# Kernel optimization log

Measured on AMD Instinct MI355X. Metric: run time of the kernel, lower is better.

Reference implementation:

```python
import jax, jax.numpy as jnp
import numpy as np

BATCH, SEQ, DIM = 4, 4096, 1024


def setup_inputs() -> dict:
    key = jax.random.key(0)
    ks = jax.random.split(key, 7)
    return {
        "x": jax.random.normal(ks[0], (BATCH, SEQ, DIM), dtype=jnp.float32),
        "hidden_r": jax.random.normal(ks[1], (BATCH, DIM), dtype=jnp.float32),
        "hidden_i": jax.random.normal(ks[2], (BATCH, DIM), dtype=jnp.float32),
        "phazor_r": jax.random.normal(ks[3], (DIM,), dtype=jnp.float32),
        "phazor_i": jax.random.normal(ks[4], (DIM,), dtype=jnp.float32),
        "phazor_init_r": jax.random.normal(ks[5], (DIM,), dtype=jnp.float32),
        "phazor_init_i": jax.random.normal(ks[6], (DIM,), dtype=jnp.float32),
    }


def reference(x, hidden_r, hidden_i, phazor_r, phazor_i, phazor_init_r, phazor_init_i):
    L = x.shape[1]
    phazor_p = phazor_r + 1j * phazor_i              # raw parameter, (dim,)
    phazor_init = phazor_init_r + 1j * phazor_init_i  # (dim,)
    hidden = hidden_r + 1j * hidden_i                 # (batch, dim)

    mag = jnp.abs(phazor_p)
    phazor = phazor_p / mag * jnp.exp(-mag)           # unit-direction * exp(-|p|), (dim,)

    # (len, dim): phazor ** t for t in [0, len)
    t = jnp.arange(L)[:, None]
    phazor_prog = phazor[None, :] ** t

    filt = phazor_prog * phazor_init[None, :]         # (len, dim)
    filt_fft = jnp.fft.fft(filt, n=2 * L, axis=0)     # (2len, dim)
    x_fft = jnp.fft.fft(x.astype(jnp.complex64), n=2 * L, axis=1)  # (batch, 2len, dim)

    conv = jnp.fft.ifft(filt_fft[None, :, :] * x_fft, axis=1)[:, :L, :]  # (batch, len, dim)

    out = conv + hidden[:, None, :] * phazor_prog[None, :, :] * phazor[None, None, :]
    return out
```

## Files before the change

kernel.cpp:

```cpp
#include <hip/hip_runtime.h>
#include <math.h>

#define BATCH 4
#define SEQ   4096
#define DIM   1024
#define VEC   4

typedef float f32x4 __attribute__((ext_vector_type(4)));

__device__ __forceinline__ void load_params4(
    const float* __restrict__ phr, const float* __restrict__ phi,
    const float* __restrict__ pir, const float* __restrict__ pii,
    int d0, float* ar, float* ai, float* br, float* bi)
{
    float4 p_r = *reinterpret_cast<const float4*>(phr + d0);
    float4 p_i = *reinterpret_cast<const float4*>(phi + d0);
    float4 q_r = *reinterpret_cast<const float4*>(pir + d0);
    float4 q_i = *reinterpret_cast<const float4*>(pii + d0);
    float prv[VEC] = {p_r.x, p_r.y, p_r.z, p_r.w};
    float piv[VEC] = {p_i.x, p_i.y, p_i.z, p_i.w};
    float qrv[VEC] = {q_r.x, q_r.y, q_r.z, q_r.w};
    float qiv[VEC] = {q_i.x, q_i.y, q_i.z, q_i.w};
#pragma unroll
    for (int j = 0; j < VEC; ++j) {
        float mag = sqrtf(prv[j] * prv[j] + piv[j] * piv[j]);
        float s = expf(-mag) / mag;
        ar[j] = prv[j] * s;
        ai[j] = piv[j] * s;
        br[j] = qrv[j];
        bi[j] = qiv[j];
    }
}

template <int NC>
__global__ __launch_bounds__(256, 4) void k_carry(
    const float* __restrict__ x,
    const float* __restrict__ phr, const float* __restrict__ phi,
    const float* __restrict__ pir, const float* __restrict__ pii,
    float2* __restrict__ carry)
{
    constexpr int S = SEQ / NC;
    const int d0 = (blockIdx.x * blockDim.x + threadIdx.x) * VEC;
    const int c = blockIdx.y, b = blockIdx.z;

    float ar[VEC], ai[VEC], br[VEC], bi[VEC];
    load_params4(phr, phi, pir, pii, d0, ar, ai, br, bi);

    const float* xp = x + ((size_t)b * SEQ + (size_t)c * S) * DIM + d0;
    float Cr[VEC] = {0.f, 0.f, 0.f, 0.f};
    float Ci[VEC] = {0.f, 0.f, 0.f, 0.f};
#pragma unroll 4
    for (int t = 0; t < S; ++t) {
        float4 xv = *reinterpret_cast<const float4*>(xp + (size_t)t * DIM);
        float xa[VEC] = {xv.x, xv.y, xv.z, xv.w};
#pragma unroll
        for (int j = 0; j < VEC; ++j) {
            float nr = fmaf(ar[j], Cr[j], fmaf(-ai[j], Ci[j], br[j] * xa[j]));
            float ni = fmaf(ar[j], Ci[j], fmaf( ai[j], Cr[j], bi[j] * xa[j]));
            Cr[j] = nr; Ci[j] = ni;
        }
    }
    float2* cp = carry + ((size_t)b * NC + c) * DIM + d0;
#pragma unroll
    for (int j = 0; j < VEC; ++j) cp[j] = make_float2(Cr[j], Ci[j]);
}

template <int NC>
__global__ __launch_bounds__(64) void k_prefix(
    const float* __restrict__ phr, const float* __restrict__ phi,
    const float* __restrict__ hr,  const float* __restrict__ hi_,
    const float2* __restrict__ carry,
    float2* __restrict__ prefix)
{
    constexpr int S = SEQ / NC;
    const int idx = blockIdx.x * blockDim.x + threadIdx.x;
    const int b = idx / DIM, d = idx % DIM;

    float pr = phr[d], pi = phi[d];
    float mag = sqrtf(pr * pr + pi * pi);
    float sc = expf(-mag) / mag;
    float ar = pr * sc, ai = pi * sc;

    float Ar = 1.f, Ai = 0.f, sr = ar, si = ai;
    int e = S;
    while (e) {
        if (e & 1) {
            float nr = Ar * sr - Ai * si;
            Ai = Ar * si + Ai * sr;
            Ar = nr;
        }
        float nr = sr * sr - si * si;
        si = 2.f * sr * si;
        sr = nr;
        e >>= 1;
    }

    float Pr = hr[idx], Pi = hi_[idx];
    constexpr int TILE = 8;
    static_assert(NC % TILE == 0, "NC must be a multiple of TILE");
    for (int base = 0; base < NC; base += TILE) {
        float2 cv[TILE];
#pragma unroll
        for (int k = 0; k < TILE; ++k)
            cv[k] = carry[((size_t)b * NC + base + k) * DIM + d];
#pragma unroll
        for (int k = 0; k < TILE; ++k) {
            prefix[((size_t)b * NC + base + k) * DIM + d] = make_float2(Pr, Pi);
            float nr = fmaf(Ar, Pr, fmaf(-Ai, Pi, cv[k].x));
            float ni = fmaf(Ar, Pi, fmaf( Ai, Pr, cv[k].y));
            Pr = nr; Pi = ni;
        }
    }
}

template <int NC, bool CPLX>
__global__ __launch_bounds__(256, 4) void k_out(
    const float* __restrict__ x,
    const float* __restrict__ phr, const float* __restrict__ phi,
    const float* __restrict__ pir, const float* __restrict__ pii,
    const float2* __restrict__ prefix,
    float* __restrict__ out)
{
    constexpr int S = SEQ / NC;
    const int d0 = (blockIdx.x * blockDim.x + threadIdx.x) * VEC;
    const int c = blockIdx.y, b = blockIdx.z;

    float ar[VEC], ai[VEC], br[VEC], bi[VEC];
    load_params4(phr, phi, pir, pii, d0, ar, ai, br, bi);

    float Cr[VEC], Ci[VEC];
    const float2* pp = prefix + ((size_t)b * NC + c) * DIM + d0;
#pragma unroll
    for (int j = 0; j < VEC; ++j) {
        float2 v = pp[j];
        Cr[j] = v.x; Ci[j] = v.y;
    }

    const float* xp = x + ((size_t)b * SEQ + (size_t)c * S) * DIM + d0;
    const size_t obase = ((size_t)b * SEQ + (size_t)c * S) * DIM + d0;
#pragma unroll 4
    for (int t = 0; t < S; ++t) {
        float4 xv = *reinterpret_cast<const float4*>(xp + (size_t)t * DIM);
        float xa[VEC] = {xv.x, xv.y, xv.z, xv.w};
#pragma unroll
        for (int j = 0; j < VEC; ++j) {
            float nr = fmaf(ar[j], Cr[j], fmaf(-ai[j], Ci[j], br[j] * xa[j]));
            float ni = fmaf(ar[j], Ci[j], fmaf( ai[j], Cr[j], bi[j] * xa[j]));
            Cr[j] = nr; Ci[j] = ni;
        }
        if (CPLX) {
            f32x4* dst = reinterpret_cast<f32x4*>(out + 2 * (obase + (size_t)t * DIM));
            f32x4 v0 = {Cr[0], Ci[0], Cr[1], Ci[1]};
            f32x4 v1 = {Cr[2], Ci[2], Cr[3], Ci[3]};
            __builtin_nontemporal_store(v0, dst);
            __builtin_nontemporal_store(v1, dst + 1);
        } else {
            f32x4* dst = reinterpret_cast<f32x4*>(out + obase + (size_t)t * DIM);
            f32x4 v0 = {Cr[0], Cr[1], Cr[2], Cr[3]};
            __builtin_nontemporal_store(v0, dst);
        }
    }
}

template <bool CPLX>
__global__ void k_serial(
    const float* __restrict__ x,
    const float* __restrict__ phr, const float* __restrict__ phi,
    const float* __restrict__ pir, const float* __restrict__ pii,
    const float* __restrict__ hr,  const float* __restrict__ hi_,
    float* __restrict__ out)
{
    const int idx = blockIdx.x * blockDim.x + threadIdx.x;
    if (idx >= BATCH * DIM) return;
    const int b = idx / DIM, d = idx % DIM;

    float pr = phr[d], pi = phi[d];
    float mag = sqrtf(pr * pr + pi * pi);
    float sc = expf(-mag) / mag;
    float ar = pr * sc, ai = pi * sc;
    float br = pir[d], bi = pii[d];

    float Cr = hr[idx], Ci = hi_[idx];
    const float* xp = x + (size_t)b * SEQ * DIM + d;
    for (int t = 0; t < SEQ; ++t) {
        float xv = xp[(size_t)t * DIM];
        float nr = fmaf(ar, Cr, fmaf(-ai, Ci, br * xv));
        float ni = fmaf(ar, Ci, fmaf( ai, Cr, bi * xv));
        Cr = nr; Ci = ni;
        size_t o = ((size_t)b * SEQ + t) * DIM + d;
        if (CPLX) {
            reinterpret_cast<float2*>(out)[o] = make_float2(Cr, Ci);
        } else {
            out[o] = Cr;
        }
    }
}

template <int NC, bool CPLX>
static void run_all(const float* x, const float* hr, const float* hi_,
                    const float* phr, const float* phi,
                    const float* pir, const float* pii,
                    float* out, void* d_ws, hipStream_t stream)
{
    float2* carry = (float2*)d_ws;
    float2* prefix = carry + (size_t)BATCH * NC * DIM;

    dim3 blk(256);
    dim3 g1(DIM / (256 * VEC), NC, BATCH);
    k_carry<NC><<<g1, blk, 0, stream>>>(x, phr, phi, pir, pii, carry);
    k_prefix<NC><<<dim3(BATCH * DIM / 64), dim3(64), 0, stream>>>(
        phr, phi, hr, hi_, carry, prefix);
    k_out<NC, CPLX><<<g1, blk, 0, stream>>>(x, phr, phi, pir, pii, prefix, out);
}

template <bool CPLX>
static void dispatch(const float* x, const float* hr, const float* hi_,
                     const float* phr, const float* phi,
                     const float* pir, const float* pii,
                     float* out, void* d_ws, size_t ws_size, hipStream_t stream)
{
    auto need = [](int nc) { return (size_t)2 * BATCH * nc * DIM * sizeof(float2); };

    if (ws_size >= need(256))
        run_all<256, CPLX>(x, hr, hi_, phr, phi, pir, pii, out, d_ws, stream);
    else if (ws_size >= need(128))
        run_all<128, CPLX>(x, hr, hi_, phr, phi, pir, pii, out, d_ws, stream);
    else if (ws_size >= need(64))
        run_all<64, CPLX>(x, hr, hi_, phr, phi, pir, pii, out, d_ws, stream);
    else if (ws_size >= need(32))
        run_all<32, CPLX>(x, hr, hi_, phr, phi, pir, pii, out, d_ws, stream);
    else if (ws_size >= need(16))
        run_all<16, CPLX>(x, hr, hi_, phr, phi, pir, pii, out, d_ws, stream);
    else
        k_serial<CPLX><<<dim3((BATCH * DIM + 255) / 256), dim3(256), 0, stream>>>(
            x, phr, phi, pir, pii, hr, hi_, out);
}

extern "C" void kernel_launch(void* const* d_in, const int* in_sizes, int n_in,
                              void* d_out, int out_size, void* d_ws, size_t ws_size,
                              hipStream_t stream) {
    const float* x   = (const float*)d_in[0];
    const float* hr  = (const float*)d_in[1];
    const float* hi_ = (const float*)d_in[2];
    const float* phr = (const float*)d_in[3];
    const float* phi = (const float*)d_in[4];
    const float* pir = (const float*)d_in[5];
    const float* pii = (const float*)d_in[6];
    float* out = (float*)d_out;

    const size_t total = (size_t)BATCH * SEQ * DIM;
    if ((size_t)out_size >= 2 * total)
        dispatch<true >(x, hr, hi_, phr, phi, pir, pii, out, d_ws, ws_size, stream);
    else
        dispatch<false>(x, hr, hi_, phr, phi, pir, pii, out, d_ws, ws_size, stream);
}
```

Baseline: 156.1 us.

## Fuse chunk-prefix scan into output kernel and fix chunk count at 128

Drops the separate prefix kernel. Each output block now recomputes its starting state by folding all earlier chunk carries with phazor^S, where S=32 is reached by five repeated squarings, and then adds the hidden term. This saves one launch and the serial prefix pass, along with the prefix buffer's write and read. In exchange, later chunks read up to 127 carries each, which adds quadratic redundant reads and compute. NC goes from 256 (when the workspace allows) to a fixed 128, and the launch-bounds occupancy hint drops to 2 blocks.

```diff
diff --git a/kernel.cpp b/kernel.cpp
--- a/kernel.cpp
+++ b/kernel.cpp
@@ -6,7 +6,11 @@
 #define DIM   1024
 #define VEC   4
 
+#define NC2 128
+#define S2  (SEQ / NC2)
+
 typedef float f32x4 __attribute__((ext_vector_type(4)));
+typedef float f32x2 __attribute__((ext_vector_type(2)));
 
 __device__ __forceinline__ void load_params4(
     const float* __restrict__ phr, const float* __restrict__ phi,
@@ -32,25 +36,23 @@
     }
 }
 
-template <int NC>
-__global__ __launch_bounds__(256, 4) void k_carry(
+__global__ __launch_bounds__(256, 2) void k1_carry(
     const float* __restrict__ x,
     const float* __restrict__ phr, const float* __restrict__ phi,
     const float* __restrict__ pir, const float* __restrict__ pii,
     float2* __restrict__ carry)
 {
-    constexpr int S = SEQ / NC;
-    const int d0 = (blockIdx.x * blockDim.x + threadIdx.x) * VEC;
-    const int c = blockIdx.y, b = blockIdx.z;
+    const int d0 = threadIdx.x * VEC;
+    const int c = blockIdx.x, b = blockIdx.y;
 
     float ar[VEC], ai[VEC], br[VEC], bi[VEC];
     load_params4(phr, phi, pir, pii, d0, ar, ai, br, bi);
 
-    const float* xp = x + ((size_t)b * SEQ + (size_t)c * S) * DIM + d0;
+    const float* xp = x + ((size_t)b * SEQ + (size_t)c * S2) * DIM + d0;
     float Cr[VEC] = {0.f, 0.f, 0.f, 0.f};
     float Ci[VEC] = {0.f, 0.f, 0.f, 0.f};
 #pragma unroll 4
-    for (int t = 0; t < S; ++t) {
+    for (int t = 0; t < S2; ++t) {
         float4 xv = *reinterpret_cast<const float4*>(xp + (size_t)t * DIM);
         float xa[VEC] = {xv.x, xv.y, xv.z, xv.w};
 #pragma unroll
@@ -60,92 +62,83 @@
             Cr[j] = nr; Ci[j] = ni;
         }
     }
-    float2* cp = carry + ((size_t)b * NC + c) * DIM + d0;
-#pragma unroll
-    for (int j = 0; j < VEC; ++j) cp[j] = make_float2(Cr[j], Ci[j]);
-}
-
-template <int NC>
-__global__ __launch_bounds__(64) void k_prefix(
-    const float* __restrict__ phr, const float* __restrict__ phi,
+    f32x4* cp = reinterpret_cast<f32x4*>(carry + ((size_t)b * NC2 + c) * DIM + d0);
+    cp[0] = f32x4{Cr[0], Ci[0], Cr[1], Ci[1]};
+    cp[1] = f32x4{Cr[2], Ci[2], Cr[3], Ci[3]};
+}
+
+template <bool CPLX>
+__global__ __launch_bounds__(256, 2) void k2_out(
+    const float* __restrict__ x,
+    const float* __restrict__ phr, const float* __restrict__ phi,
+    const float* __restrict__ pir, const float* __restrict__ pii,
     const float* __restrict__ hr,  const float* __restrict__ hi_,
     const float2* __restrict__ carry,
-    float2* __restrict__ prefix)
-{
-    constexpr int S = SEQ / NC;
-    const int idx = blockIdx.x * blockDim.x + threadIdx.x;
-    const int b = idx / DIM, d = idx % DIM;
-
-    float pr = phr[d], pi = phi[d];
-    float mag = sqrtf(pr * pr + pi * pi);
-    float sc = expf(-mag) / mag;
-    float ar = pr * sc, ai = pi * sc;
-
-    float Ar = 1.f, Ai = 0.f, sr = ar, si = ai;
-    int e = S;
-    while (e) {
-        if (e & 1) {
-            float nr = Ar * sr - Ai * si;
-            Ai = Ar * si + Ai * sr;
-            Ar = nr;
-        }
-        float nr = sr * sr - si * si;
-        si = 2.f * sr * si;
-        sr = nr;
-        e >>= 1;
-    }
-
-    float Pr = hr[idx], Pi = hi_[idx];
-    constexpr int TILE = 8;
-    static_assert(NC % TILE == 0, "NC must be a multiple of TILE");
-    for (int base = 0; base < NC; base += TILE) {
-        float2 cv[TILE];
-#pragma unroll
-        for (int k = 0; k < TILE; ++k)
-            cv[k] = carry[((size_t)b * NC + base + k) * DIM + d];
-#pragma unroll
-        for (int k = 0; k < TILE; ++k) {
-            prefix[((size_t)b * NC + base + k) * DIM + d] = make_float2(Pr, Pi);
-            float nr = fmaf(Ar, Pr, fmaf(-Ai, Pi, cv[k].x));
-            float ni = fmaf(Ar, Pi, fmaf( Ai, Pr, cv[k].y));
-            Pr = nr; Pi = ni;
-        }
-    }
-}
-
-template <int NC, bool CPLX>
-__global__ __launch_bounds__(256, 4) void k_out(
-    const float* __restrict__ x,
-    const float* __restrict__ phr, const float* __restrict__ phi,
-    const float* __restrict__ pir, const float* __restrict__ pii,
-    const float2* __restrict__ prefix,
     float* __restrict__ out)
 {
-    constexpr int S = SEQ / NC;
-    const int d0 = (blockIdx.x * blockDim.x + threadIdx.x) * VEC;
-    const int c = blockIdx.y, b = blockIdx.z;
-
-    float ar[VEC], ai[VEC], br[VEC], bi[VEC];
-    load_params4(phr, phi, pir, pii, d0, ar, ai, br, bi);
+    const int d0 = threadIdx.x * VEC;
+    const int c = blockIdx.x, b = blockIdx.y;
+
+    float ar[VEC], ai[VEC], bqr[VEC], bqi[VEC];
+    load_params4(phr, phi, pir, pii, d0, ar, ai, bqr, bqi);
+
+    float ASr[VEC], ASi[VEC];
+#pragma unroll
+    for (int j = 0; j < VEC; ++j) {
+        float sr = ar[j], si = ai[j];
+#pragma unroll
+        for (int k = 0; k < 5; ++k) {
+            float nr = sr * sr - si * si;
+            si = 2.f * sr * si;
+            sr = nr;
+        }
+        ASr[j] = sr; ASi[j] = si;
+    }
+
+    float Pr[VEC] = {0.f, 0.f, 0.f, 0.f}, Pi[VEC] = {0.f, 0.f, 0.f, 0.f};
+    float Mr[VEC] = {1.f, 1.f, 1.f, 1.f}, Mi[VEC] = {0.f, 0.f, 0.f, 0.f};
+    const float2* cb = carry + (size_t)b * NC2 * DIM + d0;
+#pragma unroll 4
+    for (int k = c - 1; k >= 0; --k) {
+        const f32x4* src = reinterpret_cast<const f32x4*>(cb + (size_t)k * DIM);
+        f32x4 g0 = src[0], g1 = src[1];
+        float gr[VEC] = {g0.x, g0.z, g1.x, g1.z};
+        float gi[VEC] = {g0.y, g0.w, g1.y, g1.w};
+#pragma unroll
+        for (int j = 0; j < VEC; ++j) {
+            Pr[j] = fmaf(Mr[j], gr[j], fmaf(-Mi[j], gi[j], Pr[j]));
+            Pi[j] = fmaf(Mr[j], gi[j], fmaf( Mi[j], gr[j], Pi[j]));
+            float nr = Mr[j] * ASr[j] - Mi[j] * ASi[j];
+            Mi[j] = Mr[j] * ASi[j] + Mi[j] * ASr[j];
+            Mr[j] = nr;
+        }
+    }
+    {
+        float4 hv_r = *reinterpret_cast<const float4*>(hr  + (size_t)b * DIM + d0);
+        float4 hv_i = *reinterpret_cast<const float4*>(hi_ + (size_t)b * DIM + d0);
+        float hrv[VEC] = {hv_r.x, hv_r.y, hv_r.z, hv_r.w};
+        float hiv[VEC] = {hv_i.x, hv_i.y, hv_i.z, hv_i.w};
+#pragma unroll
+        for (int j = 0; j < VEC; ++j) {
+            Pr[j] = fmaf(Mr[j], hrv[j], fmaf(-Mi[j], hiv[j], Pr[j]));
+            Pi[j] = fmaf(Mr[j], hiv[j], fmaf( Mi[j], hrv[j], Pi[j]));
+        }
+    }
 
     float Cr[VEC], Ci[VEC];
-    const float2* pp = prefix + ((size_t)b * NC + c) * DIM + d0;
-#pragma unroll
-    for (int j = 0; j < VEC; ++j) {
-        float2 v = pp[j];
-        Cr[j] = v.x; Ci[j] = v.y;
-    }
-
-    const float* xp = x + ((size_t)b * SEQ + (size_t)c * S) * DIM + d0;
-    const size_t obase = ((size_t)b * SEQ + (size_t)c * S) * DIM + d0;
+#pragma unroll
+    for (int j = 0; j < VEC; ++j) { Cr[j] = Pr[j]; Ci[j] = Pi[j]; }
+
+    const float* xp = x + ((size_t)b * SEQ + (size_t)c * S2) * DIM + d0;
+    const size_t obase = ((size_t)b * SEQ + (size_t)c * S2) * DIM + d0;
 #pragma unroll 4
-    for (int t = 0; t < S; ++t) {
+    for (int t = 0; t < S2; ++t) {
         float4 xv = *reinterpret_cast<const float4*>(xp + (size_t)t * DIM);
         float xa[VEC] = {xv.x, xv.y, xv.z, xv.w};
 #pragma unroll
         for (int j = 0; j < VEC; ++j) {
-            float nr = fmaf(ar[j], Cr[j], fmaf(-ai[j], Ci[j], br[j] * xa[j]));
-            float ni = fmaf(ar[j], Ci[j], fmaf( ai[j], Cr[j], bi[j] * xa[j]));
+            float nr = fmaf(ar[j], Cr[j], fmaf(-ai[j], Ci[j], bqr[j] * xa[j]));
+            float ni = fmaf(ar[j], Ci[j], fmaf( ai[j], Cr[j], bqi[j] * xa[j]));
             Cr[j] = nr; Ci[j] = ni;
         }
         if (CPLX) {
@@ -155,9 +148,9 @@
             __builtin_nontemporal_store(v0, dst);
             __builtin_nontemporal_store(v1, dst + 1);
         } else {
-            f32x4* dst = reinterpret_cast<f32x4*>(out + obase + (size_t)t * DIM);
             f32x4 v0 = {Cr[0], Cr[1], Cr[2], Cr[3]};
-            __builtin_nontemporal_store(v0, dst);
+            __builtin_nontemporal_store(
+                v0, reinterpret_cast<f32x4*>(out + obase + (size_t)t * DIM));
         }
     }
 }
@@ -196,44 +189,24 @@
     }
 }
 
-template <int NC, bool CPLX>
-static void run_all(const float* x, const float* hr, const float* hi_,
-                    const float* phr, const float* phi,
-                    const float* pir, const float* pii,
-                    float* out, void* d_ws, hipStream_t stream)
-{
-    float2* carry = (float2*)d_ws;
-    float2* prefix = carry + (size_t)BATCH * NC * DIM;
-
-    dim3 blk(256);
-    dim3 g1(DIM / (256 * VEC), NC, BATCH);
-    k_carry<NC><<<g1, blk, 0, stream>>>(x, phr, phi, pir, pii, carry);
-    k_prefix<NC><<<dim3(BATCH * DIM / 64), dim3(64), 0, stream>>>(
-        phr, phi, hr, hi_, carry, prefix);
-    k_out<NC, CPLX><<<g1, blk, 0, stream>>>(x, phr, phi, pir, pii, prefix, out);
-}
-
 template <bool CPLX>
 static void dispatch(const float* x, const float* hr, const float* hi_,
                      const float* phr, const float* phi,
                      const float* pir, const float* pii,
                      float* out, void* d_ws, size_t ws_size, hipStream_t stream)
 {
-    auto need = [](int nc) { return (size_t)2 * BATCH * nc * DIM * sizeof(float2); };
-
-    if (ws_size >= need(256))
-        run_all<256, CPLX>(x, hr, hi_, phr, phi, pir, pii, out, d_ws, stream);
-    else if (ws_size >= need(128))
-        run_all<128, CPLX>(x, hr, hi_, phr, phi, pir, pii, out, d_ws, stream);
-    else if (ws_size >= need(64))
-        run_all<64, CPLX>(x, hr, hi_, phr, phi, pir, pii, out, d_ws, stream);
-    else if (ws_size >= need(32))
-        run_all<32, CPLX>(x, hr, hi_, phr, phi, pir, pii, out, d_ws, stream);
-    else if (ws_size >= need(16))
-        run_all<16, CPLX>(x, hr, hi_, phr, phi, pir, pii, out, d_ws, stream);
-    else
+    const size_t need = (size_t)BATCH * NC2 * DIM * sizeof(float2);
+    if (ws_size >= need) {
+        float2* carry = (float2*)d_ws;
+        dim3 blk(256);
+        dim3 g(NC2, BATCH);
+        k1_carry<<<g, blk, 0, stream>>>(x, phr, phi, pir, pii, carry);
+        k2_out<CPLX><<<g, blk, 0, stream>>>(
+            x, phr, phi, pir, pii, hr, hi_, carry, out);
+    } else {
         k_serial<CPLX><<<dim3((BATCH * DIM + 255) / 256), dim3(256), 0, stream>>>(
             x, phr, phi, pir, pii, hr, hi_, out);
+    }
 }
 
 extern "C" void kernel_launch(void* const* d_in, const int* in_sizes, int n_in,
```

Measured after the change: 160.0 us. 1.03x slower.
